# Performance work log

Measured on AMD Instinct MI355X. Metric: run time of the kernel, lower is better.

## Reference

```python
import jax, jax.numpy as jnp
import numpy as np

B, T, D, L, K = 4, 2048, 2048, 2048, 4  # batch, seq, width, lru_width, conv temporal width


def setup_inputs() -> dict:
    key = jax.random.key(0)
    ks = jax.random.split(key, 12)
    s = 0.02
    f32 = jnp.float32
    return {
        "x": jax.random.normal(ks[0], (B, T, D), f32),
        "w_y": jax.random.normal(ks[1], (D, L), f32) * s,
        "b_y": jnp.zeros((L,), f32),
        "w_x": jax.random.normal(ks[2], (D, L), f32) * s,
        "b_x": jnp.zeros((L,), f32),
        "conv_w": jax.random.normal(ks[3], (K, L), f32) * s,
        "conv_b": jnp.zeros((L,), f32),
        "a_param": jax.random.uniform(ks[4], (L,), f32, 0.5, 4.0),
        "w_ig": jax.random.normal(ks[5], (L, L), f32) * s,
        "b_ig": jnp.zeros((L,), f32),
        "w_ag": jax.random.normal(ks[6], (L, L), f32) * s,
        "b_ag": jnp.zeros((L,), f32),
        "w_out": jax.random.normal(ks[7], (L, D), f32) * s,
        "b_out": jnp.zeros((D,), f32),
    }


def reference(x, w_y, b_y, w_x, b_x, conv_w, conv_b, a_param,
              w_ig, b_ig, w_ag, b_ag, w_out, b_out):
    # x: [B, T, D] (batch_first=True)
    Tn = x.shape[1]
    # gate branch: GELU(linear_y(x))
    y = jax.nn.gelu(jnp.einsum('btd,dl->btl', x, w_y) + b_y, approximate=False)
    # recurrent branch: linear_x -> causal depthwise conv1d (width K)
    xb = jnp.einsum('btd,dl->btl', x, w_x) + b_x
    xp = jnp.pad(xb, ((0, 0), (K - 1, 0), (0, 0)))  # zero left pad (fresh cache)
    conv = conv_b
    for k in range(K):  # y_t = b + sum_k w[k] * x_{t-(K-1-k)}
        conv = conv + conv_w[k] * xp[:, k:k + Tn]
    # RG-LRU
    gate_x = jax.nn.sigmoid(jnp.einsum('btl,lm->btm', conv, w_ig) + b_ig)
    gate_a = jax.nn.sigmoid(jnp.einsum('btl,lm->btm', conv, w_ag) + b_ag)
    log_a = -8.0 * gate_a * jax.nn.softplus(a_param)  # [B,T,L]
    a = jnp.exp(log_a)
    mult = jnp.sqrt(1.0 - jnp.exp(2.0 * log_a))
    reset = (jnp.arange(Tn) == 0)[None, :, None]  # reset at sequence start
    a = jnp.where(reset, 0.0, a)
    mult = jnp.where(reset, 1.0, mult)
    nx = gate_x * conv * mult
    # linear diagonal scan h_t = a_t * h_{t-1} + nx_t
    def step(h, inp):
        a_t, x_t = inp
        h = a_t * h + x_t
        return h, h
    h0 = jnp.zeros((x.shape[0], a.shape[-1]), x.dtype)
    hn, hs = jax.lax.scan(step, h0, (a.transpose(1, 0, 2), nx.transpose(1, 0, 2)))
    h_seq = hs.transpose(1, 0, 2)  # [B,T,L]
    out = jnp.einsum('btl,ld->btd', h_seq * y, w_out) + b_out
    return out, hn
```

## Files before the change

### kernel.cpp

```cpp
#include <hip/hip_runtime.h>
#include <math.h>

#define B_ 4
#define T_ 2048
#define D_ 2048
#define L_ 2048
#define KW 4
#define M_ (B_*T_)

typedef unsigned short u16;
typedef unsigned short u16x8 __attribute__((ext_vector_type(8)));
typedef __bf16 bf16x8 __attribute__((ext_vector_type(8)));
typedef float f32x4 __attribute__((ext_vector_type(4)));

__device__ __forceinline__ u16 f2bf(float f) {
    unsigned u = __float_as_uint(f);
    u += 0x7fffu + ((u >> 16) & 1u);
    return (u16)(u >> 16);
}
__device__ __forceinline__ float bf2f(u16 h) {
    return __uint_as_float(((unsigned)h) << 16);
}
__device__ __forceinline__ float gelu_exact(float v) {
    return 0.5f * v * (1.0f + erff(v * 0.70710678118654752440f));
}
__device__ __forceinline__ float sigmoidf_(float v) {
    return 1.0f / (1.0f + __expf(-v));
}
__device__ __forceinline__ void gload16(const void* g, void* l) {
    __builtin_amdgcn_global_load_lds(
        (const __attribute__((address_space(1))) void*)g,
        (__attribute__((address_space(3))) void*)l,
        16, 0, 0);
}

__global__ __launch_bounds__(256)
void castx_kernel(const float* __restrict__ in, u16* __restrict__ out)
{
    const int i = blockIdx.x * 256 + threadIdx.x;
    float4 v = ((const float4*)in)[i];
    ushort4 o;
    o.x = f2bf(v.x); o.y = f2bf(v.y); o.z = f2bf(v.z); o.w = f2bf(v.w);
    ((ushort4*)out)[i] = o;
}

__global__ __launch_bounds__(256)
void transcast_kernel(const float* __restrict__ in, u16* __restrict__ out,
                      int Kd, int Nd)
{
    __shared__ float tile[32][33];
    const int bx = blockIdx.x;
    const int by = blockIdx.y;
    const int tx = threadIdx.x & 31;
    const int ty = threadIdx.x >> 5;
    #pragma unroll
    for (int j = 0; j < 4; ++j) {
        const int r = by*32 + ty + j*8;
        tile[ty + j*8][tx] = in[(size_t)r * Nd + bx*32 + tx];
    }
    __syncthreads();
    #pragma unroll
    for (int j = 0; j < 4; ++j) {
        const int n = bx*32 + ty + j*8;
        out[(size_t)n * Kd + by*32 + tx] = f2bf(tile[tx][ty + j*8]);
    }
}

__device__ __forceinline__ void store_out(float* C, size_t idx, float v) { C[idx] = v; }
__device__ __forceinline__ void store_out(u16*   C, size_t idx, float v) { C[idx] = f2bf(v); }

#define ASLOT 16384
#define BSLOT 8192
#define AREG  (3*ASLOT)

template<int EPI, typename OutT>
__global__ __launch_bounds__(512)
void mgemm_kernel(const u16* __restrict__ A, const u16* __restrict__ BT,
                  const float* __restrict__ bias, OutT* __restrict__ C,
                  int M, int N, int K)
{
    __shared__ __align__(16) u16 lds[AREG + 3*BSLOT];

    const int tid  = threadIdx.x;
    const int wave = tid >> 6;
    const int lane = tid & 63;

    const int nbx = N >> 7;
    const int nwg = nbx * (M >> 8);
    const int bid = blockIdx.x;
    const int l   = (bid & 7) * (nwg >> 3) + (bid >> 3);
    const int bm  = (l / nbx) * 256;
    const int bn  = (l % nbx) * 128;

    const int wr = wave >> 1;
    const int wc = wave & 1;
    const int lr = lane & 15;
    const int q  = lane >> 4;
    const int sw = lane & 7;

    const int grow8 = lane >> 3;
    const int gslot = (lane & 7) ^ grow8;

    const int NT = K >> 6;

    f32x4 acc[4][4] = {};

    auto stage = [&](int tt) {
        const size_t kg = (size_t)tt << 6;
        const int slot = tt % 3;
        u16* abase = &lds[slot * ASLOT];
        u16* bbase = &lds[AREG + slot * BSLOT];
        #pragma unroll
        for (int g = 0; g < 4; ++g) {
            const int c = wave*4 + g;
            gload16(A + (size_t)(bm + c*8 + grow8) * K + kg + gslot*8,
                    &abase[c*512 + lane*8]);
        }
        #pragma unroll
        for (int g = 0; g < 2; ++g) {
            const int c = wave*2 + g;
            gload16(BT + (size_t)(bn + c*8 + grow8) * K + kg + gslot*8,
                    &bbase[c*512 + lane*8]);
        }
    };

    stage(0);
    stage(1);
    asm volatile("s_waitcnt vmcnt(6)" ::: "memory");
    __builtin_amdgcn_s_barrier();
    __builtin_amdgcn_sched_barrier(0);

    for (int t = 0; t < NT; ++t) {
        if (t + 2 < NT) stage(t + 2);

        const int slot = t % 3;
        const u16* ab = &lds[slot * ASLOT];
        const u16* bb = &lds[AREG + slot * BSLOT];

        bf16x8 af[4][2], bfr[4][2];
        #pragma unroll
        for (int i = 0; i < 4; ++i) {
            const int r = wr*64 + i*16 + lr;
            #pragma unroll
            for (int ks = 0; ks < 2; ++ks) {
                const int sk = (ks*4 + q) ^ sw;
                af[i][ks] = *(const bf16x8*)&ab[r*64 + sk*8];
            }
        }
        #pragma unroll
        for (int j = 0; j < 4; ++j) {
            const int r = wc*64 + j*16 + lr;
            #pragma unroll
            for (int ks = 0; ks < 2; ++ks) {
                const int sk = (ks*4 + q) ^ sw;
                bfr[j][ks] = *(const bf16x8*)&bb[r*64 + sk*8];
            }
        }

        __builtin_amdgcn_s_setprio(1);
        #pragma unroll
        for (int i = 0; i < 4; ++i)
            #pragma unroll
            for (int j = 0; j < 4; ++j) {
                acc[i][j] = __builtin_amdgcn_mfma_f32_16x16x32_bf16(af[i][0], bfr[j][0], acc[i][j], 0, 0, 0);
                acc[i][j] = __builtin_amdgcn_mfma_f32_16x16x32_bf16(af[i][1], bfr[j][1], acc[i][j], 0, 0, 0);
            }
        __builtin_amdgcn_s_setprio(0);

        if (t < NT - 1) {
            if (t + 2 < NT) asm volatile("s_waitcnt vmcnt(6)" ::: "memory");
            else            asm volatile("s_waitcnt vmcnt(0)" ::: "memory");
            __builtin_amdgcn_s_barrier();
            __builtin_amdgcn_sched_barrier(0);
        }
    }

    const int m0 = wr * 64;
    const int n0 = wc * 64;
    const int orow = (lane >> 4) * 4;
    #pragma unroll
    for (int i = 0; i < 4; ++i) {
        #pragma unroll
        for (int j = 0; j < 4; ++j) {
            const int col = bn + n0 + j*16 + lr;
            const float bv = bias[col];
            #pragma unroll
            for (int r = 0; r < 4; ++r) {
                const int row = bm + m0 + i*16 + orow + r;
                float v = acc[i][j][r] + bv;
                if (EPI == 1)      v = gelu_exact(v);
                else if (EPI == 2) v = sigmoidf_(v);
                store_out(C, (size_t)row * N + col, v);
            }
        }
    }
}

__global__ __launch_bounds__(256)
void conv_kernel(const u16* __restrict__ xb, const float* __restrict__ cw,
                 const float* __restrict__ cb, u16* __restrict__ out)
{
    const int idx = blockIdx.x * 256 + threadIdx.x;
    const int NL8 = L_ / 8;
    const int l = (idx % NL8) * 8;
    const int bt = idx / NL8;
    const int t = bt & (T_ - 1);
    float acc[8];
    #pragma unroll
    for (int j = 0; j < 8; ++j) acc[j] = cb[l + j];
    #pragma unroll
    for (int k = 0; k < KW; ++k) {
        const int ts = t - (KW-1) + k;
        if (ts >= 0) {
            u16x8 xv = *(const u16x8*)(xb + ((size_t)(bt - (KW-1-k))) * L_ + l);
            #pragma unroll
            for (int j = 0; j < 8; ++j)
                acc[j] = fmaf(cw[k*L_ + l + j], bf2f(xv[j]), acc[j]);
        }
    }
    u16x8 o;
    #pragma unroll
    for (int j = 0; j < 8; ++j) o[j] = f2bf(acc[j]);
    *(u16x8*)(out + (size_t)bt * L_ + l) = o;
}

__global__ __launch_bounds__(256)
void rglru_kernel(const u16* __restrict__ conv, u16* __restrict__ gxa,
                  u16* __restrict__ ganx, const float* __restrict__ ap)
{
    const int idx = blockIdx.x * 256 + threadIdx.x;
    const int NL8 = L_ / 8;
    const int l = (idx % NL8) * 8;
    const int bt = idx / NL8;
    const int t = bt & (T_ - 1);
    const size_t off = (size_t)bt * L_ + l;
    u16x8 gx = *(u16x8*)(gxa + off);
    u16x8 ga = *(u16x8*)(ganx + off);
    u16x8 cv = *(const u16x8*)(conv + off);
    u16x8 av, nxv;
    #pragma unroll
    for (int j = 0; j < 8; ++j) {
        float p  = ap[l + j];
        float sp = log1pf(expf(p));
        float la = -8.0f * bf2f(ga[j]) * sp;
        float a  = expf(la);
        float mult = sqrtf(fmaxf(0.f, 1.0f - a*a));
        if (t == 0) { a = 0.f; mult = 1.f; }
        av[j]  = f2bf(a);
        nxv[j] = f2bf(bf2f(gx[j]) * bf2f(cv[j]) * mult);
    }
    *(u16x8*)(gxa + off)  = av;
    *(u16x8*)(ganx + off) = nxv;
}

#define CHUNKS 32
#define CLEN (T_ / CHUNKS)

__global__ __launch_bounds__(256)
void scan1_kernel(const u16* __restrict__ Ab, const u16* __restrict__ Xb,
                  float* __restrict__ Pb, float* __restrict__ Sb)
{
    const int l = blockIdx.x * 256 + threadIdx.x;
    const int c = blockIdx.y;
    const int b = blockIdx.z;
    size_t base = ((size_t)b * T_ + (size_t)c * CLEN) * L_ + l;
    float h = 0.f, P = 1.f;
    #pragma unroll 4
    for (int t = 0; t < CLEN; ++t) {
        float a = bf2f(Ab[base + (size_t)t * L_]);
        float x = bf2f(Xb[base + (size_t)t * L_]);
        h = fmaf(a, h, x);
        P *= a;
    }
    const size_t o = ((size_t)b * CHUNKS + c) * L_ + l;
    Pb[o] = P;
    Sb[o] = h;
}

__global__ __launch_bounds__(256)
void scan2_kernel(const float* __restrict__ Pb, const float* __restrict__ Sb,
                  float* __restrict__ Hin, float* __restrict__ hn)
{
    const int idx = blockIdx.x * 256 + threadIdx.x;
    const int l = idx & (L_ - 1);
    const int b = idx >> 11;
    float h = 0.f;
    for (int c = 0; c < CHUNKS; ++c) {
        const size_t o = ((size_t)b * CHUNKS + c) * L_ + l;
        Hin[o] = h;
        h = fmaf(Pb[o], h, Sb[o]);
    }
    hn[(size_t)b * L_ + l] = h;
}

__global__ __launch_bounds__(256)
void scan3_kernel(const u16* __restrict__ Ab, const u16* __restrict__ Xb,
                  const float* __restrict__ Hin, const u16* __restrict__ Yb,
                  u16* __restrict__ Zb)
{
    const int l = blockIdx.x * 256 + threadIdx.x;
    const int c = blockIdx.y;
    const int b = blockIdx.z;
    float h = Hin[((size_t)b * CHUNKS + c) * L_ + l];
    size_t base = ((size_t)b * T_ + (size_t)c * CLEN) * L_ + l;
    #pragma unroll 4
    for (int t = 0; t < CLEN; ++t) {
        const size_t o = base + (size_t)t * L_;
        h = fmaf(bf2f(Ab[o]), h, bf2f(Xb[o]));
        Zb[o] = f2bf(h * bf2f(Yb[o]));
    }
}

extern "C" void kernel_launch(void* const* d_in, const int* in_sizes, int n_in,
                              void* d_out, int out_size, void* d_ws, size_t ws_size,
                              hipStream_t stream)
{
    const float* x     = (const float*)d_in[0];
    const float* w_y   = (const float*)d_in[1];
    const float* b_y   = (const float*)d_in[2];
    const float* w_x   = (const float*)d_in[3];
    const float* b_x   = (const float*)d_in[4];
    const float* cw    = (const float*)d_in[5];
    const float* cb    = (const float*)d_in[6];
    const float* ap    = (const float*)d_in[7];
    const float* w_ig  = (const float*)d_in[8];
    const float* b_ig  = (const float*)d_in[9];
    const float* w_ag  = (const float*)d_in[10];
    const float* b_ag  = (const float*)d_in[11];
    const float* w_out = (const float*)d_in[12];
    const float* b_out = (const float*)d_in[13];

    float* out = (float*)d_out;
    float* hn  = out + (size_t)M_ * D_;

    const size_t MB = 1u << 20;
    char* w = (char*)d_ws;
    u16*  xbf   = (u16*)(w + 0);
    u16*  wigb  = (u16*)(w + 0);
    u16*  wagb  = (u16*)(w + 8*MB);
    u16*  zb    = (u16*)(w + 0);
    u16*  ybf   = (u16*)(w + 32*MB);
    u16*  xbbf  = (u16*)(w + 64*MB);
    u16*  woutb = (u16*)(w + 64*MB);
    float* Pb   = (float*)(w + 72*MB);
    float* Sb   = (float*)(w + 73*MB);
    float* Hin  = (float*)(w + 74*MB);
    u16*  wyb   = (u16*)(w + 96*MB);
    u16*  wxb   = (u16*)(w + 104*MB);
    u16*  convb = (u16*)(w + 96*MB);
    u16*  gx    = (u16*)(w + 128*MB);
    u16*  ga    = (u16*)(w + 160*MB);

    const dim3 blk(256);
    const dim3 blkG(512);
    const dim3 gG((L_/128) * (M_/256));
    const dim3 gT(2048/32, 2048/32);
    const int  gE8 = (M_ * L_ / 8) / 256;
    const dim3 gScan(L_/256, CHUNKS, B_);

    hipLaunchKernelGGL(castx_kernel, dim3((M_*D_/4)/256), blk, 0, stream, x, xbf);
    hipLaunchKernelGGL(transcast_kernel, gT, blk, 0, stream, w_y, wyb, D_, L_);
    hipLaunchKernelGGL(transcast_kernel, gT, blk, 0, stream, w_x, wxb, D_, L_);
    hipLaunchKernelGGL((mgemm_kernel<1, u16>), gG, blkG, 0, stream, xbf, wyb, b_y, ybf, M_, L_, D_);
    hipLaunchKernelGGL((mgemm_kernel<0, u16>), gG, blkG, 0, stream, xbf, wxb, b_x, xbbf, M_, L_, D_);
    hipLaunchKernelGGL(transcast_kernel, gT, blk, 0, stream, w_ig, wigb, L_, L_);
    hipLaunchKernelGGL(transcast_kernel, gT, blk, 0, stream, w_ag, wagb, L_, L_);
    hipLaunchKernelGGL(conv_kernel, dim3(gE8), blk, 0, stream, xbbf, cw, cb, convb);
    hipLaunchKernelGGL(transcast_kernel, gT, blk, 0, stream, w_out, woutb, L_, D_);
    hipLaunchKernelGGL((mgemm_kernel<2, u16>), gG, blkG, 0, stream, convb, wigb, b_ig, gx, M_, L_, L_);
    hipLaunchKernelGGL((mgemm_kernel<2, u16>), gG, blkG, 0, stream, convb, wagb, b_ag, ga, M_, L_, L_);
    hipLaunchKernelGGL(rglru_kernel, dim3(gE8), blk, 0, stream, convb, gx, ga, ap);
    hipLaunchKernelGGL(scan1_kernel, gScan, blk, 0, stream, gx, ga, Pb, Sb);
    hipLaunchKernelGGL(scan2_kernel, dim3(B_*L_/256), blk, 0, stream, Pb, Sb, Hin, hn);
    hipLaunchKernelGGL(scan3_kernel, gScan, blk, 0, stream, gx, ga, Hin, ybf, zb);
    hipLaunchKernelGGL((mgemm_kernel<0, float>), gG, blkG, 0, stream, zb, woutb, b_out, out, M_, D_, L_);
}
```

Baseline: 585.4 us.

## Restructure bf16 GEMM mainloop into quadrant-interleaved double-buffered pipeline

Replaces the triple-buffered k-loop, which loaded all fragments and then issued all MFMAs, with a double-buffered schedule. Each k-tile is split into four 2x2 MFMA quadrants, and LDS fragment reads and global-to-LDS loads for half-tiles are interleaved between them, with barriers after each quadrant. Fragments for the next tile are prefetched during the last quadrant. The goal is to overlap LDS reads and global loads with MFMA work and reduce LDS footprint, at the cost of more barriers per k-tile and tricky vmcnt accounting.

```diff
diff --git a/kernel.cpp b/kernel.cpp
--- a/kernel.cpp
+++ b/kernel.cpp
@@ -33,6 +33,11 @@
         (__attribute__((address_space(3))) void*)l,
         16, 0, 0);
 }
+__device__ __forceinline__ void barf() {
+    __builtin_amdgcn_sched_barrier(0);
+    __builtin_amdgcn_s_barrier();
+    __builtin_amdgcn_sched_barrier(0);
+}
 
 __global__ __launch_bounds__(256)
 void castx_kernel(const float* __restrict__ in, u16* __restrict__ out)
@@ -69,17 +74,14 @@
 __device__ __forceinline__ void store_out(float* C, size_t idx, float v) { C[idx] = v; }
 __device__ __forceinline__ void store_out(u16*   C, size_t idx, float v) { C[idx] = f2bf(v); }
 
-#define ASLOT 16384
-#define BSLOT 8192
-#define AREG  (3*ASLOT)
-
 template<int EPI, typename OutT>
 __global__ __launch_bounds__(512)
 void mgemm_kernel(const u16* __restrict__ A, const u16* __restrict__ BT,
                   const float* __restrict__ bias, OutT* __restrict__ C,
                   int M, int N, int K)
 {
-    __shared__ __align__(16) u16 lds[AREG + 3*BSLOT];
+    __shared__ __align__(16) u16 lds[49152];
+    u16* ldsB = lds + 32768;
 
     const int tid  = threadIdx.x;
     const int wave = tid >> 6;
@@ -88,12 +90,12 @@
     const int nbx = N >> 7;
     const int nwg = nbx * (M >> 8);
     const int bid = blockIdx.x;
-    const int l   = (bid & 7) * (nwg >> 3) + (bid >> 3);
-    const int bm  = (l / nbx) * 256;
-    const int bn  = (l % nbx) * 128;
-
-    const int wr = wave >> 1;
-    const int wc = wave & 1;
+    const int li  = (bid & 7) * (nwg >> 3) + (bid >> 3);
+    const int bm  = (li / nbx) * 256;
+    const int bn  = (li % nbx) * 128;
+
+    const int wm = wave >> 1;
+    const int wn = wave & 1;
     const int lr = lane & 15;
     const int q  = lane >> 4;
     const int sw = lane & 7;
@@ -103,94 +105,125 @@
 
     const int NT = K >> 6;
 
+    const int cA0 = (wave >> 1) * 8 + (wave & 1) * 2;
+    const int cB0 = (wave >> 2) * 8 + (wave & 3);
+
+    const u16* gA0 = A  + (size_t)(bm + (cA0    )*8 + grow8) * K + gslot*8;
+    const u16* gA1 = A  + (size_t)(bm + (cA0 + 1)*8 + grow8) * K + gslot*8;
+    const u16* gA2 = A  + (size_t)(bm + (cA0 + 4)*8 + grow8) * K + gslot*8;
+    const u16* gA3 = A  + (size_t)(bm + (cA0 + 5)*8 + grow8) * K + gslot*8;
+    const u16* gB0 = BT + (size_t)(bn + (cB0    )*8 + grow8) * K + gslot*8;
+    const u16* gB1 = BT + (size_t)(bn + (cB0 + 4)*8 + grow8) * K + gslot*8;
+    const int dA0 = (cA0    )*512 + lane*8, dA1 = (cA0+1)*512 + lane*8;
+    const int dA2 = (cA0 + 4)*512 + lane*8, dA3 = (cA0+5)*512 + lane*8;
+    const int dB0 = (cB0    )*512 + lane*8, dB1 = (cB0+4)*512 + lane*8;
+
+    auto ST_AH0 = [&](int g){ u16* b = lds  + (g&1)*16384; const size_t kg = (size_t)g<<6;
+        gload16(gA0+kg, &b[dA0]); gload16(gA1+kg, &b[dA1]); };
+    auto ST_AH1 = [&](int g){ u16* b = lds  + (g&1)*16384; const size_t kg = (size_t)g<<6;
+        gload16(gA2+kg, &b[dA2]); gload16(gA3+kg, &b[dA3]); };
+    auto ST_BH0 = [&](int g){ u16* b = ldsB + (g&1)*8192;  const size_t kg = (size_t)g<<6;
+        gload16(gB0+kg, &b[dB0]); };
+    auto ST_BH1 = [&](int g){ u16* b = ldsB + (g&1)*8192;  const size_t kg = (size_t)g<<6;
+        gload16(gB1+kg, &b[dB1]); };
+
+    const int ks0 = ((    q) ^ sw) * 8;
+    const int ks1 = ((4 + q) ^ sw) * 8;
+
+    auto LD_AF = [&](const u16* Ab, int half, bf16x8 (&dst)[2][2]) {
+        #pragma unroll
+        for (int i = 0; i < 2; ++i) {
+            const int ro = (wm*64 + half*32 + i*16 + lr) * 64;
+            dst[i][0] = *(const bf16x8*)&Ab[ro + ks0];
+            dst[i][1] = *(const bf16x8*)&Ab[ro + ks1];
+        }
+    };
+    auto LD_BF = [&](const u16* Bb, int half, bf16x8 (&dst)[2][2]) {
+        #pragma unroll
+        for (int j = 0; j < 2; ++j) {
+            const int ro = (wn*64 + half*32 + j*16 + lr) * 64;
+            dst[j][0] = *(const bf16x8*)&Bb[ro + ks0];
+            dst[j][1] = *(const bf16x8*)&Bb[ro + ks1];
+        }
+    };
+
     f32x4 acc[4][4] = {};
-
-    auto stage = [&](int tt) {
-        const size_t kg = (size_t)tt << 6;
-        const int slot = tt % 3;
-        u16* abase = &lds[slot * ASLOT];
-        u16* bbase = &lds[AREG + slot * BSLOT];
-        #pragma unroll
-        for (int g = 0; g < 4; ++g) {
-            const int c = wave*4 + g;
-            gload16(A + (size_t)(bm + c*8 + grow8) * K + kg + gslot*8,
-                    &abase[c*512 + lane*8]);
-        }
-        #pragma unroll
-        for (int g = 0; g < 2; ++g) {
-            const int c = wave*2 + g;
-            gload16(BT + (size_t)(bn + c*8 + grow8) * K + kg + gslot*8,
-                    &bbase[c*512 + lane*8]);
-        }
-    };
-
-    stage(0);
-    stage(1);
-    asm volatile("s_waitcnt vmcnt(6)" ::: "memory");
-    __builtin_amdgcn_s_barrier();
-    __builtin_amdgcn_sched_barrier(0);
-
-    for (int t = 0; t < NT; ++t) {
-        if (t + 2 < NT) stage(t + 2);
-
-        const int slot = t % 3;
-        const u16* ab = &lds[slot * ASLOT];
-        const u16* bb = &lds[AREG + slot * BSLOT];
-
-        bf16x8 af[4][2], bfr[4][2];
-        #pragma unroll
-        for (int i = 0; i < 4; ++i) {
-            const int r = wr*64 + i*16 + lr;
-            #pragma unroll
-            for (int ks = 0; ks < 2; ++ks) {
-                const int sk = (ks*4 + q) ^ sw;
-                af[i][ks] = *(const bf16x8*)&ab[r*64 + sk*8];
-            }
-        }
-        #pragma unroll
-        for (int j = 0; j < 4; ++j) {
-            const int r = wc*64 + j*16 + lr;
-            #pragma unroll
-            for (int ks = 0; ks < 2; ++ks) {
-                const int sk = (ks*4 + q) ^ sw;
-                bfr[j][ks] = *(const bf16x8*)&bb[r*64 + sk*8];
-            }
-        }
-
+    bf16x8 af0[2][2], af1[2][2], bf0A[2][2], bf0B[2][2], bf1[2][2];
+
+    auto MM = [&](int mh, int nh, bf16x8 (&a)[2][2], bf16x8 (&b)[2][2]) {
         __builtin_amdgcn_s_setprio(1);
         #pragma unroll
-        for (int i = 0; i < 4; ++i)
+        for (int ks = 0; ks < 2; ++ks)
             #pragma unroll
-            for (int j = 0; j < 4; ++j) {
-                acc[i][j] = __builtin_amdgcn_mfma_f32_16x16x32_bf16(af[i][0], bfr[j][0], acc[i][j], 0, 0, 0);
-                acc[i][j] = __builtin_amdgcn_mfma_f32_16x16x32_bf16(af[i][1], bfr[j][1], acc[i][j], 0, 0, 0);
-            }
+            for (int i = 0; i < 2; ++i)
+                #pragma unroll
+                for (int j = 0; j < 2; ++j)
+                    acc[mh*2+i][nh*2+j] = __builtin_amdgcn_mfma_f32_16x16x32_bf16(
+                        a[i][ks], b[j][ks], acc[mh*2+i][nh*2+j], 0, 0, 0);
         __builtin_amdgcn_s_setprio(0);
-
-        if (t < NT - 1) {
-            if (t + 2 < NT) asm volatile("s_waitcnt vmcnt(6)" ::: "memory");
-            else            asm volatile("s_waitcnt vmcnt(0)" ::: "memory");
-            __builtin_amdgcn_s_barrier();
-            __builtin_amdgcn_sched_barrier(0);
-        }
-    }
-
-    const int m0 = wr * 64;
-    const int n0 = wc * 64;
+    };
+
+    ST_AH0(0); ST_BH1(0); ST_AH1(0); ST_BH0(0);
+    ST_AH0(1); ST_BH1(1); ST_AH1(1); ST_BH0(1);
+    asm volatile("s_waitcnt vmcnt(6)" ::: "memory");
+    barf();
+    LD_AF(lds, 0, af0);
+    LD_BF(ldsB, 0, bf0A);
+
+    auto ktile = [&](int g, bf16x8 (&bfc)[2][2], bf16x8 (&bfn)[2][2]) {
+        const u16* Ab = lds  + (g&1)*16384;
+        const u16* Bb = ldsB + (g&1)*8192;
+        const bool s1 = (g + 1 < NT), s2 = (g + 2 < NT);
+
+        LD_BF(Bb, 1, bf1);
+        MM(0, 0, af0, bfc);
+        barf();
+
+        LD_AF(Ab, 1, af1);
+        if (s2) ST_AH0(g + 2);
+        MM(0, 1, af0, bf1);
+        barf();
+
+        if (s2) ST_BH1(g + 2);
+        MM(1, 1, af1, bf1);
+        if (s1) {
+            if (s2) { asm volatile("s_waitcnt vmcnt(3)" ::: "memory"); }
+            else    { asm volatile("s_waitcnt vmcnt(0)" ::: "memory"); }
+        }
+        barf();
+
+        if (s1) {
+            const u16* AbN = lds  + ((g+1)&1)*16384;
+            const u16* BbN = ldsB + ((g+1)&1)*8192;
+            LD_AF(AbN, 0, af0);
+            LD_BF(BbN, 0, bfn);
+            if (s2) { ST_AH1(g + 2); ST_BH0(g + 2); }
+        }
+        MM(1, 0, af1, bfc);
+        barf();
+    };
+
+    for (int g = 0; g < NT; g += 2) {
+        ktile(g,     bf0A, bf0B);
+        ktile(g + 1, bf0B, bf0A);
+    }
+
     const int orow = (lane >> 4) * 4;
-    #pragma unroll
-    for (int i = 0; i < 4; ++i) {
+    float bv[4];
+    #pragma unroll
+    for (int nj = 0; nj < 4; ++nj) bv[nj] = bias[bn + wn*64 + nj*16 + lr];
+    #pragma unroll
+    for (int mi = 0; mi < 4; ++mi) {
         #pragma unroll
-        for (int j = 0; j < 4; ++j) {
-            const int col = bn + n0 + j*16 + lr;
-            const float bv = bias[col];
+        for (int r = 0; r < 4; ++r) {
+            const int row = bm + wm*64 + mi*16 + orow + r;
+            const size_t rb = (size_t)row * N + bn + wn*64 + lr;
             #pragma unroll
-            for (int r = 0; r < 4; ++r) {
-                const int row = bm + m0 + i*16 + orow + r;
-                float v = acc[i][j][r] + bv;
+            for (int nj = 0; nj < 4; ++nj) {
+                float v = acc[mi][nj][r] + bv[nj];
                 if (EPI == 1)      v = gelu_exact(v);
                 else if (EPI == 2) v = sigmoidf_(v);
-                store_out(C, (size_t)row * N + col, v);
+                store_out(C, rb + nj*16, v);
             }
         }
     }
```

New measurement: 577.3 us. No clear change (-1.4%).
